# Kernel optimization log

Hardware: AMD Instinct MI355X
Metric: run time of the kernel (lower is better)

Reference implementation:

```python
import jax, jax.numpy as jnp
import numpy as np
from jax import lax

GAMMA = 0.99
LAM = 0.95
CLIP_PARAM = 0.2
VALUE_LOSS_COEF = 0.5
ENTROPY_COEF = 0.01
EPS = 1e-09

B, T = 4096, 2048


def setup_inputs() -> dict:
    key = jax.random.key(0)
    ks = jax.random.split(key, 6)
    rewards = jax.random.normal(ks[0], (B, T), dtype=jnp.float32)
    values = jax.random.normal(ks[1], (B, T + 1), dtype=jnp.float32)
    ref_probs = jax.random.uniform(ks[2], (B, T), dtype=jnp.float32)
    old_probs = jax.random.uniform(ks[3], (B, T), dtype=jnp.float32)
    curr_probs = jax.random.uniform(ks[4], (B, T), dtype=jnp.float32)
    # episode-continuation masks: mostly 1, occasional 0 (episode boundary)
    masks = (jax.random.uniform(ks[5], (B, T)) > 0.02).astype(jnp.float32)
    return {"rewards": rewards, "values": values, "ref_probs": ref_probs,
            "old_probs": old_probs, "curr_probs": curr_probs, "masks": masks}


def compute_gae(rewards, values, masks, gamma, lam):
    # single fused reverse scan over time; per-step state is (B,)
    def step(carry, xs):
        r, v, v_next, m = xs
        delta = r + gamma * v_next * m - v
        adv = delta + gamma * lam * m * carry
        return adv, adv

    xs = (rewards.T, values[:, :-1].T, values[:, 1:].T, masks.T)  # each (T, B)
    _, advs = lax.scan(step, jnp.zeros(rewards.shape[0], rewards.dtype), xs, reverse=True)
    advantages = advs.T  # (B, T)
    returns = advantages + values[:, :-1]
    return advantages, returns


def reference(rewards, values, ref_probs, old_probs, curr_probs, masks):
    advantages, returns = compute_gae(rewards, values, masks, GAMMA, LAM)
    # torch .std() is unbiased (ddof=1)
    advantages = (advantages - advantages.mean()) / (advantages.std(ddof=1) + EPS)
    ratios = curr_probs / (old_probs + EPS)
    surr1 = ratios * advantages
    surr2 = jnp.clip(ratios, 1.0 - CLIP_PARAM, 1.0 + CLIP_PARAM) * advantages
    ppo_loss = -jnp.minimum(surr1, surr2).mean()
    value_loss = jnp.mean((returns - values[:, :-1]) ** 2)
    entropy_loss = -jnp.mean(curr_probs * jnp.log(curr_probs + EPS))
    total_loss = ppo_loss + VALUE_LOSS_COEF * value_loss + ENTROPY_COEF * entropy_loss
    return (total_loss, ppo_loss, VALUE_LOSS_COEF * value_loss, ENTROPY_COEF * entropy_loss)
```

## Files before the change

### kernel.cpp

```cpp
#include <hip/hip_runtime.h>
#include <math.h>


#define GAMMA     0.99f
#define LAM       0.95f
#define CLIP_LO   0.8f
#define CLIP_HI   1.2f
#define EPSF      1e-9f

constexpr int BB = 4096;
constexpr int TT = 2048;
constexpr long long NN = (long long)BB * TT;
constexpr int GAE_BLOCKS = BB / 2;
constexpr int PPO_BLOCKS = 4096;

struct Stats { float mean; float inv; double sum2; };
static constexpr size_t GAE_PART_OFF = 64;
static constexpr size_t PPO_PART_OFF = GAE_PART_OFF + GAE_BLOCKS * sizeof(float2);
static constexpr size_t ADV_OFF      = PPO_PART_OFF + PPO_BLOCKS * sizeof(float2);

__device__ __forceinline__ unsigned bf16_rne(float x) {
    unsigned u = __float_as_uint(x);
    u += 0x7FFFu + ((u >> 16) & 1u);
    return u >> 16;
}

__global__ __launch_bounds__(256, 4) void gae_kernel(
    const float* __restrict__ rewards,
    const float* __restrict__ values,
    const float* __restrict__ masks,
    uint4* __restrict__ advb,
    float2* __restrict__ partials)
{
    const int tid  = threadIdx.x;
    const int lane = tid & 63;
    const int wave = tid >> 6;
    const int t0   = tid * 8;
    const int row0 = blockIdx.x * 2;
    const int row1 = row0 + 1;

    __shared__ float2 wTa[4], wTb[4];
    __shared__ float  wr1[4], wr2[4];

    const float* ra = rewards + (size_t)row0 * TT;
    const float* ma = masks   + (size_t)row0 * TT;
    const float* rb = rewards + (size_t)row1 * TT;
    const float* mb = masks   + (size_t)row1 * TT;

    const size_t vwA = (size_t)row0 * (TT + 1);
    const size_t vwB = (size_t)row1 * (TT + 1);
    const int ofsA = (int)(vwA & 3);
    const int ofsB = (int)(vwB & 3);
    const float4* vA4 = (const float4*)(values + (vwA & ~(size_t)3));
    const float4* vB4 = (const float4*)(values + (vwB & ~(size_t)3));

    float4 ra0 = *(const float4*)(ra + t0);
    float4 ra1 = *(const float4*)(ra + t0 + 4);
    float4 ma0 = *(const float4*)(ma + t0);
    float4 ma1 = *(const float4*)(ma + t0 + 4);
    float4 rb0 = *(const float4*)(rb + t0);
    float4 rb1 = *(const float4*)(rb + t0 + 4);
    float4 mb0 = *(const float4*)(mb + t0);
    float4 mb1 = *(const float4*)(mb + t0 + 4);
    float4 fa0 = vA4[2 * tid];
    float4 fa1 = vA4[2 * tid + 1];
    float4 fa2 = vA4[2 * tid + 2];
    float4 fb0 = vB4[2 * tid];
    float4 fb1 = vB4[2 * tid + 1];
    float4 fb2 = vB4[2 * tid + 2];

    float va[9], vb[9];
    {
        float f[12] = {fa0.x, fa0.y, fa0.z, fa0.w, fa1.x, fa1.y, fa1.z, fa1.w,
                       fa2.x, fa2.y, fa2.z, fa2.w};
        if (ofsA == 0) {
#pragma unroll
            for (int j = 0; j < 9; ++j) va[j] = f[j];
        } else {
#pragma unroll
            for (int j = 0; j < 9; ++j) va[j] = f[j + 2];
        }
    }
    {
        float f[12] = {fb0.x, fb0.y, fb0.z, fb0.w, fb1.x, fb1.y, fb1.z, fb1.w,
                       fb2.x, fb2.y, fb2.z, fb2.w};
        if (ofsB == 1) {
#pragma unroll
            for (int j = 0; j < 9; ++j) vb[j] = f[j + 1];
        } else {
#pragma unroll
            for (int j = 0; j < 9; ++j) vb[j] = f[j + 3];
        }
    }

    float rA[8] = {ra0.x, ra0.y, ra0.z, ra0.w, ra1.x, ra1.y, ra1.z, ra1.w};
    float mA[8] = {ma0.x, ma0.y, ma0.z, ma0.w, ma1.x, ma1.y, ma1.z, ma1.w};
    float rB[8] = {rb0.x, rb0.y, rb0.z, rb0.w, rb1.x, rb1.y, rb1.z, rb1.w};
    float mB[8] = {mb0.x, mb0.y, mb0.z, mb0.w, mb1.x, mb1.y, mb1.z, mb1.w};

    float laA[8], SA[8], laB[8], SB[8];
    {
        float d[8], c[8];
#pragma unroll
        for (int j = 0; j < 8; ++j) {
            d[j] = rA[j] + GAMMA * va[j + 1] * mA[j] - va[j];
            c[j] = (GAMMA * LAM) * mA[j];
        }
        laA[7] = d[7]; SA[7] = c[7];
#pragma unroll
        for (int j = 6; j >= 0; --j) { laA[j] = d[j] + c[j] * laA[j + 1]; SA[j] = c[j] * SA[j + 1]; }
    }
    {
        float d[8], c[8];
#pragma unroll
        for (int j = 0; j < 8; ++j) {
            d[j] = rB[j] + GAMMA * vb[j + 1] * mB[j] - vb[j];
            c[j] = (GAMMA * LAM) * mB[j];
        }
        laB[7] = d[7]; SB[7] = c[7];
#pragma unroll
        for (int j = 6; j >= 0; --j) { laB[j] = d[j] + c[j] * laB[j + 1]; SB[j] = c[j] * SB[j + 1]; }
    }

    float Aa = SA[0], Ba = laA[0];
    float Ab = SB[0], Bb = laB[0];
#pragma unroll
    for (int d = 1; d < 64; d <<= 1) {
        float A2a = __shfl_down(Aa, d, 64), B2a = __shfl_down(Ba, d, 64);
        float A2b = __shfl_down(Ab, d, 64), B2b = __shfl_down(Bb, d, 64);
        if (lane + d < 64) {
            Ba = Ba + Aa * B2a;  Aa = Aa * A2a;
            Bb = Bb + Ab * B2b;  Ab = Ab * A2b;
        }
    }
    if (lane == 0) { wTa[wave] = make_float2(Aa, Ba); wTb[wave] = make_float2(Ab, Bb); }
    __syncthreads();
    float Ca = 0.0f, Cb = 0.0f;
    for (int ww = 3; ww > wave; --ww) {
        Ca = wTa[ww].y + wTa[ww].x * Ca;
        Cb = wTb[ww].y + wTb[ww].x * Cb;
    }
    float A1a = __shfl_down(Aa, 1, 64), B1a = __shfl_down(Ba, 1, 64);
    float A1b = __shfl_down(Ab, 1, 64), B1b = __shfl_down(Bb, 1, 64);
    float carA = (lane < 63) ? (B1a + A1a * Ca) : Ca;
    float carB = (lane < 63) ? (B1b + A1b * Cb) : Cb;

    float s1 = 0.f, s2 = 0.f;
    unsigned ha[8], hb[8];
#pragma unroll
    for (int j = 0; j < 8; ++j) {
        float a = laA[j] + SA[j] * carA;
        s1 += a; s2 += a * a;
        ha[j] = bf16_rne(a);
        float b = laB[j] + SB[j] * carB;
        s1 += b; s2 += b * b;
        hb[j] = bf16_rne(b);
    }
    uint4 pa = {ha[0] | (ha[1] << 16), ha[2] | (ha[3] << 16),
                ha[4] | (ha[5] << 16), ha[6] | (ha[7] << 16)};
    uint4 pb = {hb[0] | (hb[1] << 16), hb[2] | (hb[3] << 16),
                hb[4] | (hb[5] << 16), hb[6] | (hb[7] << 16)};
    advb[row0 * 256 + tid] = pa;
    advb[row1 * 256 + tid] = pb;

#pragma unroll
    for (int off = 32; off > 0; off >>= 1) {
        s1 += __shfl_down(s1, off, 64);
        s2 += __shfl_down(s2, off, 64);
    }
    if (lane == 0) { wr1[wave] = s1; wr2[wave] = s2; }
    __syncthreads();
    if (tid == 0) {
        float2 p = {wr1[0] + wr1[1] + wr1[2] + wr1[3],
                    wr2[0] + wr2[1] + wr2[2] + wr2[3]};
        partials[blockIdx.x] = p;
    }
}

__global__ __launch_bounds__(256) void finalize_stats(
    const float2* __restrict__ gp, Stats* __restrict__ stats)
{
    const int tid = threadIdx.x;
    __shared__ double l1[256], l2[256];
    double s1 = 0.0, s2 = 0.0;
    for (int i = tid; i < GAE_BLOCKS; i += 256) {
        float2 p = gp[i];
        s1 += (double)p.x;
        s2 += (double)p.y;
    }
    l1[tid] = s1; l2[tid] = s2;
    __syncthreads();
    for (int st = 128; st > 0; st >>= 1) {
        if (tid < st) { l1[tid] += l1[tid + st]; l2[tid] += l2[tid + st]; }
        __syncthreads();
    }
    if (tid == 0) {
        double S1 = l1[0], S2 = l2[0];
        double mean = S1 / (double)NN;
        double var  = (S2 - S1 * S1 / (double)NN) / (double)(NN - 1);
        stats->mean = (float)mean;
        stats->inv  = (float)(1.0 / (sqrt(var) + 1e-9));
        stats->sum2 = S2;
    }
}

__global__ __launch_bounds__(256, 8) void ppo_kernel(
    const float* __restrict__ adv_bf16,
    const float* __restrict__ oldp,
    const float* __restrict__ currp,
    const Stats* __restrict__ stats,
    float2* __restrict__ partials)
{
    const float mean = stats->mean;
    const float inv  = stats->inv;
    const int tid = threadIdx.x;
    const int g   = blockIdx.x * 256 + tid;

    const uint4*  a4 = (const uint4*)adv_bf16;
    const float4* o4 = (const float4*)oldp;
    const float4* c4 = (const float4*)currp;

    uint4  A  = a4[g];
    float4 O0 = o4[2 * g], O1 = o4[2 * g + 1];
    float4 C0 = c4[2 * g], C1 = c4[2 * g + 1];

    float av[8] = {__uint_as_float(A.x << 16), __uint_as_float(A.x & 0xFFFF0000u),
                   __uint_as_float(A.y << 16), __uint_as_float(A.y & 0xFFFF0000u),
                   __uint_as_float(A.z << 16), __uint_as_float(A.z & 0xFFFF0000u),
                   __uint_as_float(A.w << 16), __uint_as_float(A.w & 0xFFFF0000u)};
    float ov[8] = {O0.x, O0.y, O0.z, O0.w, O1.x, O1.y, O1.z, O1.w};
    float cv[8] = {C0.x, C0.y, C0.z, C0.w, C1.x, C1.y, C1.z, C1.w};

    float sm = 0.f, se = 0.f;
#pragma unroll
    for (int j = 0; j < 8; ++j) {
        float an    = (av[j] - mean) * inv;
        float ratio = cv[j] * __builtin_amdgcn_rcpf(ov[j] + EPSF);
        float rc    = fminf(fmaxf(ratio, CLIP_LO), CLIP_HI);
        sm += fminf(ratio * an, rc * an);
        se += cv[j] * __logf(cv[j] + EPSF);
    }

#pragma unroll
    for (int off = 32; off > 0; off >>= 1) {
        sm += __shfl_down(sm, off, 64);
        se += __shfl_down(se, off, 64);
    }
    __shared__ float w1[4], w2[4];
    const int wave = tid >> 6, lane = tid & 63;
    if (lane == 0) { w1[wave] = sm; w2[wave] = se; }
    __syncthreads();
    if (tid == 0) {
        float2 p = {w1[0] + w1[1] + w1[2] + w1[3],
                    w2[0] + w2[1] + w2[2] + w2[3]};
        partials[blockIdx.x] = p;
    }
}

__global__ __launch_bounds__(256) void finalize_out(
    const float2* __restrict__ pp,
    const Stats* __restrict__ stats,
    float* __restrict__ out)
{
    const int tid = threadIdx.x;
    __shared__ double l1[256], l2[256];
    double s1 = 0.0, s2 = 0.0;
    for (int i = tid; i < PPO_BLOCKS; i += 256) {
        float2 p = pp[i];
        s1 += (double)p.x;
        s2 += (double)p.y;
    }
    l1[tid] = s1; l2[tid] = s2;
    __syncthreads();
    for (int st = 128; st > 0; st >>= 1) {
        if (tid < st) { l1[tid] += l1[tid + st]; l2[tid] += l2[tid + st]; }
        __syncthreads();
    }
    if (tid == 0) {
        double invN = 1.0 / (double)NN;
        double vl   = 0.5  * (stats->sum2 * invN);
        double ppo  = -(l1[0] * invN);
        double ent  = -0.01 * (l2[0] * invN);
        out[0] = (float)(ppo + vl + ent);
        out[1] = (float)ppo;
        out[2] = (float)vl;
        out[3] = (float)ent;
    }
}

extern "C" void kernel_launch(void* const* d_in, const int* in_sizes, int n_in,
                              void* d_out, int out_size, void* d_ws, size_t ws_size,
                              hipStream_t stream) {
    const float* rewards = (const float*)d_in[0];
    const float* values  = (const float*)d_in[1];
    const float* oldp    = (const float*)d_in[3];
    const float* currp   = (const float*)d_in[4];
    const float* masks   = (const float*)d_in[5];

    Stats*  stats = (Stats*)d_ws;
    float2* gaep  = (float2*)((char*)d_ws + GAE_PART_OFF);
    float2* ppop  = (float2*)((char*)d_ws + PPO_PART_OFF);
    uint4*  advb  = (uint4*)((char*)d_ws + ADV_OFF);
    float*  out   = (float*)d_out;

    gae_kernel<<<GAE_BLOCKS, 256, 0, stream>>>(rewards, values, masks, advb, gaep);
    finalize_stats<<<1, 256, 0, stream>>>(gaep, stats);
    ppo_kernel<<<PPO_BLOCKS, 256, 0, stream>>>((const float*)advb, oldp, currp, stats, ppop);
    finalize_out<<<1, 256, 0, stream>>>(ppop, stats, out);
}
```

Measured before the change: 206.2 us.

## Process eight rows per GAE block with software-pipelined row prefetch

The GAE kernel now gives each block eight rows instead of two, launching 512 blocks. It double-buffers row loads in registers so the next row's rewards, masks and values are fetched while the current row's scan runs, with sched barriers to keep that ordering. The intent is to hide global-load latency and amortise per-block overhead. In exchange there are fewer blocks in flight and a lower launch-bounds occupancy hint, which could reduce memory-level parallelism on a bandwidth-bound kernel.

```diff
diff --git a/kernel.cpp b/kernel.cpp
--- a/kernel.cpp
+++ b/kernel.cpp
@@ -11,7 +11,8 @@
 constexpr int BB = 4096;
 constexpr int TT = 2048;
 constexpr long long NN = (long long)BB * TT;
-constexpr int GAE_BLOCKS = BB / 2;
+constexpr int GAE_BLOCKS = 512;
+constexpr int ROWS_PER_BLOCK = 8;
 constexpr int PPO_BLOCKS = 4096;
 
 struct Stats { float mean; float inv; double sum2; };
@@ -25,7 +26,73 @@
     return u >> 16;
 }
 
-__global__ __launch_bounds__(256, 4) void gae_kernel(
+#define LOADROW(r, R0, R1, M0, M1, F0, F1, F2) do {                         \
+    const float* _rp = rewards + (size_t)(r) * TT;                          \
+    const float* _mp = masks   + (size_t)(r) * TT;                          \
+    const size_t _vw = (size_t)(r) * (TT + 1);                              \
+    const float4* _v4 = (const float4*)(values + (_vw & ~(size_t)3));       \
+    R0 = *(const float4*)(_rp + t0);                                        \
+    R1 = *(const float4*)(_rp + t0 + 4);                                    \
+    M0 = *(const float4*)(_mp + t0);                                        \
+    M1 = *(const float4*)(_mp + t0 + 4);                                    \
+    F0 = _v4[2 * tid];                                                      \
+    F1 = _v4[2 * tid + 1];                                                  \
+    F2 = _v4[2 * tid + 2];                                                  \
+} while (0)
+
+#define COMPUTE(r, PAR, R0, R1, M0, M1, F0, F1, F2) do {                    \
+    float rr[8] = {R0.x, R0.y, R0.z, R0.w, R1.x, R1.y, R1.z, R1.w};         \
+    float mm[8] = {M0.x, M0.y, M0.z, M0.w, M1.x, M1.y, M1.z, M1.w};         \
+    float ff[12] = {F0.x, F0.y, F0.z, F0.w, F1.x, F1.y, F1.z, F1.w,         \
+                    F2.x, F2.y, F2.z, F2.w};                                \
+    float vv[9];                                                            \
+    const int _ofs = (int)((r) & 3);                      \
+    if (_ofs == 0) {                                                        \
+        _Pragma("unroll") for (int j = 0; j < 9; ++j) vv[j] = ff[j];        \
+    } else if (_ofs == 1) {                                                 \
+        _Pragma("unroll") for (int j = 0; j < 9; ++j) vv[j] = ff[j + 1];    \
+    } else if (_ofs == 2) {                                                 \
+        _Pragma("unroll") for (int j = 0; j < 9; ++j) vv[j] = ff[j + 2];    \
+    } else {                                                                \
+        _Pragma("unroll") for (int j = 0; j < 9; ++j) vv[j] = ff[j + 3];    \
+    }                                                                       \
+    float la[8], S[8];                                                      \
+    {                                                                       \
+        float d[8], c[8];                                                   \
+        _Pragma("unroll") for (int j = 0; j < 8; ++j) {                     \
+            d[j] = rr[j] + GAMMA * vv[j + 1] * mm[j] - vv[j];               \
+            c[j] = (GAMMA * LAM) * mm[j];                                   \
+        }                                                                   \
+        la[7] = d[7]; S[7] = c[7];                                          \
+        _Pragma("unroll") for (int j = 6; j >= 0; --j) {                    \
+            la[j] = d[j] + c[j] * la[j + 1];                                \
+            S[j]  = c[j] * S[j + 1];                                        \
+        }                                                                   \
+    }                                                                       \
+    float A = S[0], Bv = la[0];                                             \
+    _Pragma("unroll") for (int d2 = 1; d2 < 64; d2 <<= 1) {                 \
+        float A2 = __shfl_down(A, d2, 64), B2 = __shfl_down(Bv, d2, 64);    \
+        if (lane + d2 < 64) { Bv = Bv + A * B2; A = A * A2; }               \
+    }                                                                       \
+    if (lane == 0) wT[PAR][wave] = make_float2(A, Bv);                      \
+    __syncthreads();                                                        \
+    float C = 0.f;                                                          \
+    for (int ww = 3; ww > wave; --ww)                                       \
+        C = wT[PAR][ww].y + wT[PAR][ww].x * C;                              \
+    float A1 = __shfl_down(A, 1, 64), B1 = __shfl_down(Bv, 1, 64);          \
+    float car = (lane < 63) ? (B1 + A1 * C) : C;                            \
+    unsigned hh[8];                                                         \
+    _Pragma("unroll") for (int j = 0; j < 8; ++j) {                         \
+        float a = la[j] + S[j] * car;                                       \
+        s1 += a; s2 += a * a;                                               \
+        hh[j] = bf16_rne(a);                                                \
+    }                                                                       \
+    uint4 pk = {hh[0] | (hh[1] << 16), hh[2] | (hh[3] << 16),               \
+                hh[4] | (hh[5] << 16), hh[6] | (hh[7] << 16)};              \
+    advb[(size_t)(r) * 256 + tid] = pk;                                     \
+} while (0)
+
+__global__ __launch_bounds__(256, 2) void gae_kernel(
     const float* __restrict__ rewards,
     const float* __restrict__ values,
     const float* __restrict__ masks,
@@ -36,132 +103,29 @@
     const int lane = tid & 63;
     const int wave = tid >> 6;
     const int t0   = tid * 8;
-    const int row0 = blockIdx.x * 2;
-    const int row1 = row0 + 1;
-
-    __shared__ float2 wTa[4], wTb[4];
+    const int rbase = blockIdx.x * ROWS_PER_BLOCK;
+
+    __shared__ float2 wT[2][4];
     __shared__ float  wr1[4], wr2[4];
 
-    const float* ra = rewards + (size_t)row0 * TT;
-    const float* ma = masks   + (size_t)row0 * TT;
-    const float* rb = rewards + (size_t)row1 * TT;
-    const float* mb = masks   + (size_t)row1 * TT;
-
-    const size_t vwA = (size_t)row0 * (TT + 1);
-    const size_t vwB = (size_t)row1 * (TT + 1);
-    const int ofsA = (int)(vwA & 3);
-    const int ofsB = (int)(vwB & 3);
-    const float4* vA4 = (const float4*)(values + (vwA & ~(size_t)3));
-    const float4* vB4 = (const float4*)(values + (vwB & ~(size_t)3));
-
-    float4 ra0 = *(const float4*)(ra + t0);
-    float4 ra1 = *(const float4*)(ra + t0 + 4);
-    float4 ma0 = *(const float4*)(ma + t0);
-    float4 ma1 = *(const float4*)(ma + t0 + 4);
-    float4 rb0 = *(const float4*)(rb + t0);
-    float4 rb1 = *(const float4*)(rb + t0 + 4);
-    float4 mb0 = *(const float4*)(mb + t0);
-    float4 mb1 = *(const float4*)(mb + t0 + 4);
-    float4 fa0 = vA4[2 * tid];
-    float4 fa1 = vA4[2 * tid + 1];
-    float4 fa2 = vA4[2 * tid + 2];
-    float4 fb0 = vB4[2 * tid];
-    float4 fb1 = vB4[2 * tid + 1];
-    float4 fb2 = vB4[2 * tid + 2];
-
-    float va[9], vb[9];
-    {
-        float f[12] = {fa0.x, fa0.y, fa0.z, fa0.w, fa1.x, fa1.y, fa1.z, fa1.w,
-                       fa2.x, fa2.y, fa2.z, fa2.w};
-        if (ofsA == 0) {
-#pragma unroll
-            for (int j = 0; j < 9; ++j) va[j] = f[j];
-        } else {
-#pragma unroll
-            for (int j = 0; j < 9; ++j) va[j] = f[j + 2];
-        }
-    }
-    {
-        float f[12] = {fb0.x, fb0.y, fb0.z, fb0.w, fb1.x, fb1.y, fb1.z, fb1.w,
-                       fb2.x, fb2.y, fb2.z, fb2.w};
-        if (ofsB == 1) {
-#pragma unroll
-            for (int j = 0; j < 9; ++j) vb[j] = f[j + 1];
-        } else {
-#pragma unroll
-            for (int j = 0; j < 9; ++j) vb[j] = f[j + 3];
-        }
-    }
-
-    float rA[8] = {ra0.x, ra0.y, ra0.z, ra0.w, ra1.x, ra1.y, ra1.z, ra1.w};
-    float mA[8] = {ma0.x, ma0.y, ma0.z, ma0.w, ma1.x, ma1.y, ma1.z, ma1.w};
-    float rB[8] = {rb0.x, rb0.y, rb0.z, rb0.w, rb1.x, rb1.y, rb1.z, rb1.w};
-    float mB[8] = {mb0.x, mb0.y, mb0.z, mb0.w, mb1.x, mb1.y, mb1.z, mb1.w};
-
-    float laA[8], SA[8], laB[8], SB[8];
-    {
-        float d[8], c[8];
-#pragma unroll
-        for (int j = 0; j < 8; ++j) {
-            d[j] = rA[j] + GAMMA * va[j + 1] * mA[j] - va[j];
-            c[j] = (GAMMA * LAM) * mA[j];
-        }
-        laA[7] = d[7]; SA[7] = c[7];
-#pragma unroll
-        for (int j = 6; j >= 0; --j) { laA[j] = d[j] + c[j] * laA[j + 1]; SA[j] = c[j] * SA[j + 1]; }
-    }
-    {
-        float d[8], c[8];
-#pragma unroll
-        for (int j = 0; j < 8; ++j) {
-            d[j] = rB[j] + GAMMA * vb[j + 1] * mB[j] - vb[j];
-            c[j] = (GAMMA * LAM) * mB[j];
-        }
-        laB[7] = d[7]; SB[7] = c[7];
-#pragma unroll
-        for (int j = 6; j >= 0; --j) { laB[j] = d[j] + c[j] * laB[j + 1]; SB[j] = c[j] * SB[j + 1]; }
-    }
-
-    float Aa = SA[0], Ba = laA[0];
-    float Ab = SB[0], Bb = laB[0];
-#pragma unroll
-    for (int d = 1; d < 64; d <<= 1) {
-        float A2a = __shfl_down(Aa, d, 64), B2a = __shfl_down(Ba, d, 64);
-        float A2b = __shfl_down(Ab, d, 64), B2b = __shfl_down(Bb, d, 64);
-        if (lane + d < 64) {
-            Ba = Ba + Aa * B2a;  Aa = Aa * A2a;
-            Bb = Bb + Ab * B2b;  Ab = Ab * A2b;
-        }
-    }
-    if (lane == 0) { wTa[wave] = make_float2(Aa, Ba); wTb[wave] = make_float2(Ab, Bb); }
-    __syncthreads();
-    float Ca = 0.0f, Cb = 0.0f;
-    for (int ww = 3; ww > wave; --ww) {
-        Ca = wTa[ww].y + wTa[ww].x * Ca;
-        Cb = wTb[ww].y + wTb[ww].x * Cb;
-    }
-    float A1a = __shfl_down(Aa, 1, 64), B1a = __shfl_down(Ba, 1, 64);
-    float A1b = __shfl_down(Ab, 1, 64), B1b = __shfl_down(Bb, 1, 64);
-    float carA = (lane < 63) ? (B1a + A1a * Ca) : Ca;
-    float carB = (lane < 63) ? (B1b + A1b * Cb) : Cb;
-
     float s1 = 0.f, s2 = 0.f;
-    unsigned ha[8], hb[8];
-#pragma unroll
-    for (int j = 0; j < 8; ++j) {
-        float a = laA[j] + SA[j] * carA;
-        s1 += a; s2 += a * a;
-        ha[j] = bf16_rne(a);
-        float b = laB[j] + SB[j] * carB;
-        s1 += b; s2 += b * b;
-        hb[j] = bf16_rne(b);
-    }
-    uint4 pa = {ha[0] | (ha[1] << 16), ha[2] | (ha[3] << 16),
-                ha[4] | (ha[5] << 16), ha[6] | (ha[7] << 16)};
-    uint4 pb = {hb[0] | (hb[1] << 16), hb[2] | (hb[3] << 16),
-                hb[4] | (hb[5] << 16), hb[6] | (hb[7] << 16)};
-    advb[row0 * 256 + tid] = pa;
-    advb[row1 * 256 + tid] = pb;
+
+    float4 aR0, aR1, aM0, aM1, aF0, aF1, aF2;
+    float4 bR0, bR1, bM0, bM1, bF0, bF1, bF2;
+
+    LOADROW(rbase, aR0, aR1, aM0, aM1, aF0, aF1, aF2);
+
+#pragma unroll 1
+    for (int k2 = 0; k2 < ROWS_PER_BLOCK / 2; ++k2) {
+        const int r0 = rbase + 2 * k2;
+        LOADROW(r0 + 1, bR0, bR1, bM0, bM1, bF0, bF1, bF2);
+        __builtin_amdgcn_sched_barrier(0);
+        COMPUTE(r0, 0, aR0, aR1, aM0, aM1, aF0, aF1, aF2);
+        const int rn = (k2 < ROWS_PER_BLOCK / 2 - 1) ? (r0 + 2) : r0;
+        LOADROW(rn, aR0, aR1, aM0, aM1, aF0, aF1, aF2);
+        __builtin_amdgcn_sched_barrier(0);
+        COMPUTE(r0 + 1, 1, bR0, bR1, bM0, bM1, bF0, bF1, bF2);
+    }
 
 #pragma unroll
     for (int off = 32; off > 0; off >>= 1) {
@@ -171,9 +135,8 @@
     if (lane == 0) { wr1[wave] = s1; wr2[wave] = s2; }
     __syncthreads();
     if (tid == 0) {
-        float2 p = {wr1[0] + wr1[1] + wr1[2] + wr1[3],
-                    wr2[0] + wr2[1] + wr2[2] + wr2[3]};
-        partials[blockIdx.x] = p;
+        partials[blockIdx.x] = make_float2(wr1[0] + wr1[1] + wr1[2] + wr1[3],
+                                           wr2[0] + wr2[1] + wr2[2] + wr2[3]);
     }
 }
 
```

Measured after the change: 204.6 us. No clear change (-0.8%).
